# Performance work log

Hardware: AMD Instinct MI355X
Metric: run time of the kernel (lower is better)

## Reference

```python
import jax, jax.numpy as jnp
import numpy as np

H = 2048       # hidden_size
F = 1024       # moe_intermediate_size
E = 32         # n_routed_experts
G = 8          # n_group
TOPK_GROUP = 3
TOP_K = 6      # num_experts_per_tok
N_SHARED = 2
SCALE = 1.0    # routed_scaling_factor
B, S = 1, 2048


def setup_inputs() -> dict:
    key = jax.random.key(0)
    ks = jax.random.split(key, 8)
    std = 0.02
    return {
        "hidden_states": jax.random.normal(ks[0], (B, S, H), dtype=jnp.float32),
        "w_gate": jax.random.normal(ks[1], (E, H), dtype=jnp.float32) * std,
        "wg": jax.random.normal(ks[2], (E, H, F), dtype=jnp.float32) * std,  # stacked gate_proj
        "wu": jax.random.normal(ks[3], (E, H, F), dtype=jnp.float32) * std,  # stacked up_proj
        "wd": jax.random.normal(ks[4], (E, F, H), dtype=jnp.float32) * std,  # stacked down_proj
        "sg": jax.random.normal(ks[5], (N_SHARED * F, H), dtype=jnp.float32) * std,  # shared gate_proj
        "su": jax.random.normal(ks[6], (N_SHARED * F, H), dtype=jnp.float32) * std,  # shared up_proj
        "sd": jax.random.normal(ks[7], (H, N_SHARED * F), dtype=jnp.float32) * std,  # shared down_proj
    }


def reference(hidden_states, w_gate, wg, wu, wd, sg, su, sd):
    b, s, h = hidden_states.shape
    x = hidden_states.reshape(-1, h)                    # [T, H]
    T = x.shape[0]

    # ---- MoEGate (softmax scoring, group_limited_greedy top-k) ----
    logits = x.astype(jnp.float32) @ w_gate.T           # [T, E]
    scores = jax.nn.softmax(logits, axis=-1)
    group_scores = scores.reshape(T, G, E // G).max(axis=-1)          # [T, G]
    _, group_idx = jax.lax.top_k(group_scores, TOPK_GROUP)            # [T, topk_group]
    group_mask = jax.nn.one_hot(group_idx, G, dtype=scores.dtype).sum(axis=1)  # [T, G]
    score_mask = jnp.repeat(group_mask, E // G, axis=-1)              # [T, E]
    tmp_scores = jnp.where(score_mask > 0.5, scores, 0.0)
    topk_weight, topk_idx = jax.lax.top_k(tmp_scores, TOP_K)          # [T, K]
    # norm_topk_prob=True, top_k>1
    topk_weight = topk_weight / (topk_weight.sum(axis=-1, keepdims=True) + 1e-20) * SCALE

    # combine weights per (token, expert): scatter topk weights (indices distinct)
    combine_w = jnp.zeros((T, E), dtype=jnp.float32)
    combine_w = combine_w.at[jnp.arange(T)[:, None], topk_idx].add(topk_weight)

    # ---- routed experts: dense grouped GEMMs, weighted combine ----
    g = jnp.einsum('th,ehf->etf', x, wg)                # [E, T, F]
    u = jnp.einsum('th,ehf->etf', x, wu)                # [E, T, F]
    act = jax.nn.silu(g) * u                            # SiLU gated
    act = act * combine_w.T[:, :, None]                 # fold combine weights before down-proj
    y = jnp.einsum('etf,efh->th', act, wd)              # [T, H]

    # ---- shared experts ----
    shared = (jax.nn.silu(x @ sg.T) * (x @ su.T)) @ sd.T

    return (y + shared).reshape(b, s, h)
```

## Files before the change

### kernel.cpp

```cpp
#include <hip/hip_runtime.h>

#define HD   2048
#define FD   1024
#define NEXP 32
#define TOPK 6
#define TT   2048
#define SDIM 2048
#define NPAIR (TT*TOPK)

typedef __bf16 bf16x8 __attribute__((ext_vector_type(8)));
typedef float  f32x4  __attribute__((ext_vector_type(4)));

#define GLOAD_LDS16(g, l) __builtin_amdgcn_global_load_lds( \
    (const __attribute__((address_space(1))) void*)(g),     \
    (__attribute__((address_space(3))) void*)(l), 16, 0, 0)

#define WAIT_VM3  asm volatile("s_waitcnt vmcnt(3)" ::: "memory")
#define WAIT_VM0  asm volatile("s_waitcnt vmcnt(0)" ::: "memory")
#define BAR() do { __builtin_amdgcn_s_barrier(); } while (0)

__device__ __forceinline__ ushort f2b(float f) {
  __bf16 h = (__bf16)f;
  union { __bf16 h; ushort u; } v; v.h = h;
  return v.u;
// ... 102 lines not shown

__global__ __launch_bounds__(256) void fconv4(
    const float* __restrict__ s0, const float* __restrict__ s1,
    const float* __restrict__ s2, const float* __restrict__ s3,
    ushort* __restrict__ d0, ushort* __restrict__ d1,
    ushort* __restrict__ d2, ushort* __restrict__ d3)
{
  int sel = blockIdx.y;
  const float* in = (sel == 0) ? s0 : (sel == 1) ? s1 : (sel == 2) ? s2 : s3;
  ushort* out = (sel == 0) ? d0 : (sel == 1) ? d1 : (sel == 2) ? d2 : d3;
  int i = blockIdx.x * blockDim.x + threadIdx.x;
  float4 v = ((const float4*)in)[i];
  ((ushort4*)out)[i] = make_ushort4(f2b(v.x), f2b(v.y), f2b(v.z), f2b(v.w));
}

#define TSTR 76
__global__ __launch_bounds__(256) void tconv2(
    const float* __restrict__ in0, const float* __restrict__ in1,
    ushort* __restrict__ out0, ushort* __restrict__ out1, int R, int C)
{
  __shared__ ushort T[64*TSTR];
  const float* inz = blockIdx.z ? in1 : in0;
  ushort* outz = blockIdx.z ? out1 : out0;
  int tiles_c = C >> 6;
  int bt = blockIdx.x;
  int r0 = (bt / tiles_c) << 6;
  int c0 = (bt % tiles_c) << 6;
  const float* src = inz + (size_t)blockIdx.y * R * C;
  ushort* dst = outz + (size_t)blockIdx.y * R * C;
  int t = threadIdx.x;
  int row = (t >> 4) << 2;
  int col4 = (t & 15) << 2;
  float vv[4][4];
  #pragma unroll
  for (int i = 0; i < 4; ++i) {
    float4 v = *(const float4*)(src + (size_t)(r0 + row + i) * C + c0 + col4);
    vv[i][0] = v.x; vv[i][1] = v.y; vv[i][2] = v.z; vv[i][3] = v.w;
  }
  #pragma unroll
  for (int cc = 0; cc < 4; ++cc)
    *(ushort4*)&T[(col4 + cc)*TSTR + row] =
      make_ushort4(f2b(vv[0][cc]), f2b(vv[1][cc]), f2b(vv[2][cc]), f2b(vv[3][cc]));
  __syncthreads();
  #pragma unroll
  for (int p = 0; p < 2; ++p) {
    int item = t + p*256;
    int oc = item >> 3, seg = item & 7;
    ushort4 a = *(const ushort4*)&T[oc*TSTR + seg*8];
    ushort4 b = *(const ushort4*)&T[oc*TSTR + seg*8 + 4];
    ushort* d = dst + (size_t)(c0 + oc) * R + r0 + seg*8;
    *(ushort4*)(d)     = a;
    *(ushort4*)(d + 4) = b;
  }
}

__global__ __launch_bounds__(256) void combine_kernel(
    const ushort* __restrict__ pairout, const int* __restrict__ inv, float* __restrict__ y)
{
  int t = blockIdx.x;
  int h0 = threadIdx.x * 8;
  const int* iv = inv + t*TOPK;
  float* yr = y + (size_t)t * HD + h0;
  float4 y0 = *(const float4*)(yr);
  float4 y1 = *(const float4*)(yr + 4);
  float acc[8] = {y0.x, y0.y, y0.z, y0.w, y1.x, y1.y, y1.z, y1.w};
  #pragma unroll
  for (int r = 0; r < TOPK; ++r) {
    int p = iv[r];
    const ushort* pr = pairout + (size_t)p * HD + h0;
    ushort4 a = *(const ushort4*)(pr);
    ushort4 b = *(const ushort4*)(pr + 4);
    acc[0] += b2f(a.x); acc[1] += b2f(a.y); acc[2] += b2f(a.z); acc[3] += b2f(a.w);
    acc[4] += b2f(b.x); acc[5] += b2f(b.y); acc[6] += b2f(b.z); acc[7] += b2f(b.w);
  }
  *(float4*)(yr)     = make_float4(acc[0], acc[1], acc[2], acc[3]);
  *(float4*)(yr + 4) = make_float4(acc[4], acc[5], acc[6], acc[7]);
}


__global__ __launch_bounds__(512, 4) void gu_routed_b(
    const ushort* __restrict__ xb, const ushort* __restrict__ wgt, const ushort* __restrict__ wut,
    const int* __restrict__ pair_tok, const float* __restrict__ pair_w,
    const int* __restrict__ cnt, const int* __restrict__ offs,
    const int* __restrict__ tl_e, const int* __restrict__ tl_m, const int* __restrict__ ntl,
    ushort* __restrict__ act)
{
  __shared__ ushort A[3][256*32];
  __shared__ ushort Bg[3][64*32];
  __shared__ ushort Bu[3][64*32];

  int nact = ntl[0] * 16;
  int bid = blockIdx.x;
  if (bid >= nact) return;
  int wid = xcd_swz(bid, nact);
  int tile = wid >> 4;
  int nt = wid & 15;
  int e  = tl_e[tile];
  int m0 = tl_m[tile];
  int ce = cnt[e];
  int oe = offs[e];
  int n0 = nt * 64;
  int tid = threadIdx.x, lane = tid & 63, w = tid >> 6;

  int csrc = (lane & 3) ^ ((lane >> 3) & 3);
  const ushort* asrc[2];
  #pragma unroll
  for (int j = 0; j < 2; ++j) {
    int r = (2*w + j)*16 + (lane >> 2);
    int pi = min(m0 + r, ce - 1);
    asrc[j] = xb + (size_t)pair_tok[oe + pi] * HD + csrc * 8;
  }
  int tsel = w >> 2;
  int bw = w & 3;
  const ushort* bsrc = (tsel ? wut : wgt) +
      ((size_t)e * FD + n0 + bw*16 + (lane >> 2)) * HD + csrc * 8;
  ushort* bdst0 = tsel ? &Bu[0][bw*512] : &Bg[0][bw*512];
  ushort* bdst1 = tsel ? &Bu[1][bw*512] : &Bg[1][bw*512];
  ushort* bdst2 = tsel ? &Bu[2][bw*512] : &Bg[2][bw*512];

  int lm = lane & 15, lg = lane >> 4;
  int wr = w >> 1, wc = w & 1;
  int asw = (lm >> 1) & 3;

  f32x4 accg[4][2], accu[4][2];
  #pragma unroll
  for (int m = 0; m < 4; ++m)
    #pragma unroll
    for (int n = 0; n < 2; ++n) { accg[m][n] = f32x4{0,0,0,0}; accu[m][n] = f32x4{0,0,0,0}; }

  #define GUB_ISSUE(T, BUF, BD) do { \
    GLOAD_LDS16(asrc[0] + (T)*32, &A[BUF][(2*w)*512]); \
    GLOAD_LDS16(asrc[1] + (T)*32, &A[BUF][(2*w+1)*512]); \
    GLOAD_LDS16(bsrc + (T)*32, BD); \
  } while (0)
  #define GUB_COMPUTE(BUF) do { \
    bf16x8 a[4], bg[2], bu[2]; \
    _Pragma("unroll") \
    for (int m = 0; m < 4; ++m) \
      a[m] = *(const bf16x8*)&A[BUF][(wr*64 + m*16 + lm)*32 + (lg ^ asw)*8]; \
    _Pragma("unroll") \
    for (int n = 0; n < 2; ++n) { \
      int row = wc*32 + n*16 + lm; \
      bg[n] = *(const bf16x8*)&Bg[BUF][row*32 + (lg ^ asw)*8]; \
      bu[n] = *(const bf16x8*)&Bu[BUF][row*32 + (lg ^ asw)*8]; \
    } \
    __builtin_amdgcn_s_setprio(1); \
    _Pragma("unroll") \
    for (int m = 0; m < 4; ++m) \
      _Pragma("unroll") \
      for (int n = 0; n < 2; ++n) { \
        accg[m][n] = __builtin_amdgcn_mfma_f32_16x16x32_bf16(a[m], bg[n], accg[m][n], 0, 0, 0); \
        accu[m][n] = __builtin_amdgcn_mfma_f32_16x16x32_bf16(a[m], bu[n], accu[m][n], 0, 0, 0); \
      } \
    __builtin_amdgcn_s_setprio(0); \
  } while (0)

  GUB_ISSUE(0, 0, bdst0);
  GUB_ISSUE(1, 1, bdst1);
  WAIT_VM3;
  BAR();

  for (int tt = 0; tt < 20; ++tt) {
    int t = tt * 3;
    GUB_ISSUE(t+2, 2, bdst2); GUB_COMPUTE(0); WAIT_VM3; BAR();
    GUB_ISSUE(t+3, 0, bdst0); GUB_COMPUTE(1); WAIT_VM3; BAR();
    GUB_ISSUE(t+4, 1, bdst1); GUB_COMPUTE(2); WAIT_VM3; BAR();
  }
  GUB_ISSUE(62, 2, bdst2); GUB_COMPUTE(0); WAIT_VM3; BAR();
  GUB_ISSUE(63, 0, bdst0); GUB_COMPUTE(1); WAIT_VM3; BAR();
  GUB_COMPUTE(2); WAIT_VM0; BAR();
  GUB_COMPUTE(0);
  #undef GUB_ISSUE
  #undef GUB_COMPUTE

  #pragma unroll
  for (int m = 0; m < 4; ++m) {
    #pragma unroll
    for (int j = 0; j < 4; ++j) {
      int rl = wr*64 + m*16 + lg*4 + j;
      int pi = m0 + rl;
      if (pi >= ce) continue;
      float pwv = pair_w[oe + pi];
      size_t base = (size_t)(oe + pi) * FD + n0 + wc*32;
      #pragma unroll
      for (int n = 0; n < 2; ++n) {
        float gv = accg[m][n][j];
        float uv = accu[m][n][j];
        float sv = gv / (1.f + __expf(-gv));
        act[base + n*16 + lm] = f2b(sv * uv * pwv);
      }
    }
  }
}

__global__ __launch_bounds__(512, 4) void down_routed_b(
    const ushort* __restrict__ act, const ushort* __restrict__ wdt,
    const int* __restrict__ cnt, const int* __restrict__ offs,
    const int* __restrict__ tl_e, const int* __restrict__ tl_m, const int* __restrict__ ntl,
    ushort* __restrict__ pairout)
{
  __shared__ ushort A[3][256*32];
  __shared__ ushort Bd[3][128*32];

  int nact = ntl[0] * 16;
  int bid = blockIdx.x;
  if (bid >= nact) return;
  int wid = xcd_swz(bid, nact);
  int tile = wid >> 4;
  int nt = wid & 15;
  int e  = tl_e[tile];
  int m0 = tl_m[tile];
  int ce = cnt[e];
  int oe = offs[e];
  int n0 = nt * 128;
  int tid = threadIdx.x, lane = tid & 63, w = tid >> 6;

  int csrc = (lane & 3) ^ ((lane >> 3) & 3);
  const ushort* asrc[2];
  #pragma unroll
  for (int j = 0; j < 2; ++j) {
    int r = (2*w + j)*16 + (lane >> 2);
    int pi = min(m0 + r, ce - 1);
    asrc[j] = act + (size_t)(oe + pi) * FD + csrc * 8;
  }
  const ushort* bsrc = wdt + ((size_t)e * HD + n0 + w*16 + (lane >> 2)) * FD + csrc * 8;

  int lm = lane & 15, lg = lane >> 4;
  int wr = w >> 1, wc = w & 1;
  int asw = (lm >> 1) & 3;

  f32x4 acc[4][4];
  #pragma unroll
  for (int m = 0; m < 4; ++m)
    #pragma unroll
    for (int n = 0; n < 4; ++n) acc[m][n] = f32x4{0,0,0,0};

  #define DNB_ISSUE(T, BUF) do { \
    GLOAD_LDS16(asrc[0] + (T)*32, &A[BUF][(2*w)*512]); \
    GLOAD_LDS16(asrc[1] + (T)*32, &A[BUF][(2*w+1)*512]); \
    GLOAD_LDS16(bsrc + (T)*32, &Bd[BUF][w*512]); \
  } while (0)
  #define DNB_COMPUTE(BUF) do { \
    bf16x8 a[4], b[4]; \
    _Pragma("unroll") \
    for (int m = 0; m < 4; ++m) \
      a[m] = *(const bf16x8*)&A[BUF][(wr*64 + m*16 + lm)*32 + (lg ^ asw)*8]; \
    _Pragma("unroll") \
    for (int n = 0; n < 4; ++n) { \
      int row = wc*64 + n*16 + lm; \
      b[n] = *(const bf16x8*)&Bd[BUF][row*32 + (lg ^ asw)*8]; \
    } \
    __builtin_amdgcn_s_setprio(1); \
    _Pragma("unroll") \
    for (int m = 0; m < 4; ++m) \
      _Pragma("unroll") \
      for (int n = 0; n < 4; ++n) \
        acc[m][n] = __builtin_amdgcn_mfma_f32_16x16x32_bf16(a[m], b[n], acc[m][n], 0, 0, 0); \
    __builtin_amdgcn_s_setprio(0); \
  } while (0)

  DNB_ISSUE(0, 0);
  DNB_ISSUE(1, 1);
  WAIT_VM3;
  BAR();

  for (int tt = 0; tt < 10; ++tt) {
    int t = tt * 3;
    DNB_ISSUE(t+2, 2); DNB_COMPUTE(0); WAIT_VM3; BAR();
    DNB_ISSUE(t+3, 0); DNB_COMPUTE(1); WAIT_VM3; BAR();
    DNB_ISSUE(t+4, 1); DNB_COMPUTE(2); WAIT_VM3; BAR();
  }
  DNB_COMPUTE(0); WAIT_VM0; BAR();
  DNB_COMPUTE(1);
  #undef DNB_ISSUE
  #undef DNB_COMPUTE

  #pragma unroll
  for (int m = 0; m < 4; ++m) {
    #pragma unroll
    for (int j = 0; j < 4; ++j) {
      int rl = wr*64 + m*16 + lg*4 + j;
      int pi = m0 + rl;
      if (pi >= ce) continue;
      size_t base = (size_t)(oe + pi) * HD + n0 + wc*64;
      #pragma unroll
      for (int n = 0; n < 4; ++n)
        pairout[base + n*16 + lm] = f2b(acc[m][n][j]);
    }
  }
}

__global__ __launch_bounds__(512, 4) void shared_gu_b(
    const ushort* __restrict__ xb, const ushort* __restrict__ sgb, const ushort* __restrict__ sub,
    ushort* __restrict__ sact)
{
  __shared__ ushort A[3][256*32];
  __shared__ ushort Bg[3][64*32];
  __shared__ ushort Bu[3][64*32];

  int bid = blockIdx.x;
  int wid = (bid & 7) * 32 + (bid >> 3);
  int mt = wid & 7;
  int nt = wid >> 3;
  int m0 = mt * 256;
  int n0 = nt * 64;
  int tid = threadIdx.x, lane = tid & 63, w = tid >> 6;

  int csrc = (lane & 3) ^ ((lane >> 3) & 3);
  const ushort* asrc[2];
  #pragma unroll
  for (int j = 0; j < 2; ++j) {
    int r = (2*w + j)*16 + (lane >> 2);
    asrc[j] = xb + (size_t)(m0 + r) * HD + csrc * 8;
  }
  int tsel = w >> 2;
  int bw = w & 3;
  const ushort* bsrc = (tsel ? sub : sgb) + (size_t)(n0 + bw*16 + (lane >> 2)) * HD + csrc * 8;
  ushort* bdst0 = tsel ? &Bu[0][bw*512] : &Bg[0][bw*512];
  ushort* bdst1 = tsel ? &Bu[1][bw*512] : &Bg[1][bw*512];
  ushort* bdst2 = tsel ? &Bu[2][bw*512] : &Bg[2][bw*512];

  int lm = lane & 15, lg = lane >> 4;
  int wr = w >> 1, wc = w & 1;
  int asw = (lm >> 1) & 3;

  f32x4 accg[4][2], accu[4][2];
  #pragma unroll
  for (int m = 0; m < 4; ++m)
    #pragma unroll
    for (int n = 0; n < 2; ++n) { accg[m][n] = f32x4{0,0,0,0}; accu[m][n] = f32x4{0,0,0,0}; }

  #define SGB_ISSUE(T, BUF, BD) do { \
    GLOAD_LDS16(asrc[0] + (T)*32, &A[BUF][(2*w)*512]); \
    GLOAD_LDS16(asrc[1] + (T)*32, &A[BUF][(2*w+1)*512]); \
    GLOAD_LDS16(bsrc + (T)*32, BD); \
  } while (0)
  #define SGB_COMPUTE(BUF) do { \
    bf16x8 a[4], bg[2], bu[2]; \
    _Pragma("unroll") \
    for (int m = 0; m < 4; ++m) \
      a[m] = *(const bf16x8*)&A[BUF][(wr*64 + m*16 + lm)*32 + (lg ^ asw)*8]; \
    _Pragma("unroll") \
    for (int n = 0; n < 2; ++n) { \
      int row = wc*32 + n*16 + lm; \
      bg[n] = *(const bf16x8*)&Bg[BUF][row*32 + (lg ^ asw)*8]; \
      bu[n] = *(const bf16x8*)&Bu[BUF][row*32 + (lg ^ asw)*8]; \
    } \
    __builtin_amdgcn_s_setprio(1); \
    _Pragma("unroll") \
    for (int m = 0; m < 4; ++m) \
      _Pragma("unroll") \
      for (int n = 0; n < 2; ++n) { \
        accg[m][n] = __builtin_amdgcn_mfma_f32_16x16x32_bf16(a[m], bg[n], accg[m][n], 0, 0, 0); \
        accu[m][n] = __builtin_amdgcn_mfma_f32_16x16x32_bf16(a[m], bu[n], accu[m][n], 0, 0, 0); \
      } \
    __builtin_amdgcn_s_setprio(0); \
  } while (0)

  SGB_ISSUE(0, 0, bdst0);
  SGB_ISSUE(1, 1, bdst1);
  WAIT_VM3;
  BAR();

  for (int tt = 0; tt < 20; ++tt) {
    int t = tt * 3;
    SGB_ISSUE(t+2, 2, bdst2); SGB_COMPUTE(0); WAIT_VM3; BAR();
    SGB_ISSUE(t+3, 0, bdst0); SGB_COMPUTE(1); WAIT_VM3; BAR();
    SGB_ISSUE(t+4, 1, bdst1); SGB_COMPUTE(2); WAIT_VM3; BAR();
  }
  SGB_ISSUE(62, 2, bdst2); SGB_COMPUTE(0); WAIT_VM3; BAR();
  SGB_ISSUE(63, 0, bdst0); SGB_COMPUTE(1); WAIT_VM3; BAR();
  SGB_COMPUTE(2); WAIT_VM0; BAR();
  SGB_COMPUTE(0);
  #undef SGB_ISSUE
  #undef SGB_COMPUTE

  #pragma unroll
  for (int m = 0; m < 4; ++m) {
    #pragma unroll
    for (int j = 0; j < 4; ++j) {
      int rl = wr*64 + m*16 + lg*4 + j;
      size_t base = (size_t)(m0 + rl) * SDIM + n0 + wc*32;
      #pragma unroll
      for (int n = 0; n < 2; ++n) {
        float gv = accg[m][n][j];
        float uv = accu[m][n][j];
        float sv = gv / (1.f + __expf(-gv));
        sact[base + n*16 + lm] = f2b(sv * uv);
      }
    }
  }
}

__global__ __launch_bounds__(512, 4) void shared_down_b(
    const ushort* __restrict__ sact, const ushort* __restrict__ sdb, float* __restrict__ y)
{
  __shared__ ushort A[3][256*32];
  __shared__ ushort Bd[3][128*32];

  int bid = blockIdx.x;
  int wid = (bid & 7) * 16 + (bid >> 3);
  int mt = wid & 7;
  int nt = wid >> 3;
  int m0 = mt * 256;
  int n0 = nt * 128;
  int tid = threadIdx.x, lane = tid & 63, w = tid >> 6;

  int csrc = (lane & 3) ^ ((lane >> 3) & 3);
  const ushort* asrc[2];
  #pragma unroll
  for (int j = 0; j < 2; ++j) {
    int r = (2*w + j)*16 + (lane >> 2);
    asrc[j] = sact + (size_t)(m0 + r) * SDIM + csrc * 8;
  }
  const ushort* bsrc = sdb + (size_t)(n0 + w*16 + (lane >> 2)) * SDIM + csrc * 8;

  int lm = lane & 15, lg = lane >> 4;
  int wr = w >> 1, wc = w & 1;
  int asw = (lm >> 1) & 3;

  f32x4 acc[4][4];
  #pragma unroll
  for (int m = 0; m < 4; ++m)
    #pragma unroll
    for (int n = 0; n < 4; ++n) acc[m][n] = f32x4{0,0,0,0};

  #define SDB_ISSUE(T, BUF) do { \
    GLOAD_LDS16(asrc[0] + (T)*32, &A[BUF][(2*w)*512]); \
    GLOAD_LDS16(asrc[1] + (T)*32, &A[BUF][(2*w+1)*512]); \
    GLOAD_LDS16(bsrc + (T)*32, &Bd[BUF][w*512]); \
  } while (0)
  #define SDB_COMPUTE(BUF) do { \
    bf16x8 a[4], b[4]; \
    _Pragma("unroll") \
    for (int m = 0; m < 4; ++m) \
      a[m] = *(const bf16x8*)&A[BUF][(wr*64 + m*16 + lm)*32 + (lg ^ asw)*8]; \
    _Pragma("unroll") \
    for (int n = 0; n < 4; ++n) { \
      int row = wc*64 + n*16 + lm; \
      b[n] = *(const bf16x8*)&Bd[BUF][row*32 + (lg ^ asw)*8]; \
    } \
    __builtin_amdgcn_s_setprio(1); \
    _Pragma("unroll") \
    for (int m = 0; m < 4; ++m) \
      _Pragma("unroll") \
      for (int n = 0; n < 4; ++n) \
        acc[m][n] = __builtin_amdgcn_mfma_f32_16x16x32_bf16(a[m], b[n], acc[m][n], 0, 0, 0); \
    __builtin_amdgcn_s_setprio(0); \
  } while (0)

  SDB_ISSUE(0, 0);
  SDB_ISSUE(1, 1);
  WAIT_VM3;
  BAR();

  for (int tt = 0; tt < 20; ++tt) {
    int t = tt * 3;
    SDB_ISSUE(t+2, 2); SDB_COMPUTE(0); WAIT_VM3; BAR();
    SDB_ISSUE(t+3, 0); SDB_COMPUTE(1); WAIT_VM3; BAR();
    SDB_ISSUE(t+4, 1); SDB_COMPUTE(2); WAIT_VM3; BAR();
  }
  SDB_ISSUE(62, 2); SDB_COMPUTE(0); WAIT_VM3; BAR();
  SDB_ISSUE(63, 0); SDB_COMPUTE(1); WAIT_VM3; BAR();
  SDB_COMPUTE(2); WAIT_VM0; BAR();
  SDB_COMPUTE(0);
  #undef SDB_ISSUE
  #undef SDB_COMPUTE

  #pragma unroll
  for (int m = 0; m < 4; ++m) {
    #pragma unroll
    for (int j = 0; j < 4; ++j) {
      int rl = wr*64 + m*16 + lg*4 + j;
      size_t base = (size_t)(m0 + rl) * HD + n0 + wc*64;
      #pragma unroll
      for (int n = 0; n < 4; ++n)
        y[base + n*16 + lm] = acc[m][n][j];
    }
  }
}

extern "C" void kernel_launch(void* const* d_in, const int* in_sizes, int n_in,
                              void* d_out, int out_size, void* d_ws, size_t ws_size,
                              hipStream_t stream) {
  const float* x     = (const float*)d_in[0];
  const float* wgate = (const float*)d_in[1];
  const float* wg    = (const float*)d_in[2];
  const float* wu    = (const float*)d_in[3];
  const float* wd    = (const float*)d_in[4];
  const float* sg    = (const float*)d_in[5];
  const float* su    = (const float*)d_in[6];
  const float* sd    = (const float*)d_in[7];
// ... 17 lines not shown
  ushort* wgt  = (ushort*)(ws + 50331648);
  ushort* wut  = (ushort*)(ws + 184549376);
  ushort* wdt  = (ushort*)(ws + 318767104);
  ushort* sgb  = (ushort*)(ws + 452984832);
  ushort* sub  = (ushort*)(ws + 461373440);
  ushort* sdb  = (ushort*)(ws + 469762048);
  ushort* pairout = wgt;

  hipMemsetAsync(cnt, 0, 512, stream);

  gating_kernel<<<dim3(TT), dim3(64), 0, stream>>>(x, wgate, tidx, tw, cnt);
  scan_kernel<<<dim3(1), dim3(64), 0, stream>>>(cnt, offs, tl_e, tl_m, ntl);
  fill_kernel<<<dim3(48), dim3(256), 0, stream>>>(tidx, tw, offs, curc, ptok, pw, inv);

  fconv4<<<dim3(4096, 4), dim3(256), 0, stream>>>(x, sg, su, sd, xb, sgb, sub, sdb);
  tconv2<<<dim3(512, NEXP, 2), dim3(256), 0, stream>>>(wg, wu, wgt, wut, HD, FD);
  tconv2<<<dim3(512, NEXP, 1), dim3(256), 0, stream>>>(wd, wd, wdt, wdt, FD, HD);

  shared_gu_b<<<dim3(256), dim3(512), 0, stream>>>(xb, sgb, sub, sact);
  shared_down_b<<<dim3(128), dim3(512), 0, stream>>>(sact, sdb, y);
  gu_routed_b<<<dim3(1280), dim3(512), 0, stream>>>(xb, wgt, wut, ptok, pw, cnt, offs,
                                                    tl_e, tl_m, ntl, act);
  down_routed_b<<<dim3(1280), dim3(512), 0, stream>>>(act, wdt, cnt, offs,
                                                      tl_e, tl_m, ntl, pairout);
  combine_kernel<<<dim3(TT), dim3(256), 0, stream>>>(pairout, inv, y);
}
```

Measured before the change: 733.4 us.

## Merge routed/shared GEMMs and wd transpose into heterogeneous mega kernels

Fuses the routed gate/up GEMM, the wd transpose-convert and the shared gate/up GEMM into one launch that dispatches on block index. The routed and shared down GEMMs are likewise merged into a second launch, and the wg/wu transposes now run two jobs per 512-thread block. The aim is to overlap independent memory-bound conversion with compute-bound GEMMs, cut launch gaps, and fill the tail of the routed grid. In exchange, each block holds a union-sized shared pool and register use is set by the heaviest branch, which can lower occupancy for the light transpose blocks.

```diff
diff --git a/kernel.cpp b/kernel.cpp
--- a/kernel.cpp
+++ b/kernel.cpp
@@ -7,6 +7,7 @@
 #define TT   2048
 #define SDIM 2048
 #define NPAIR (TT*TOPK)
+#define TSTR 76
 
 typedef __bf16 bf16x8 __attribute__((ext_vector_type(8)));
 typedef float  f32x4  __attribute__((ext_vector_type(4)));
@@ -140,21 +141,15 @@
   ((ushort4*)out)[i] = make_ushort4(f2b(v.x), f2b(v.y), f2b(v.z), f2b(v.w));
 }
 
-#define TSTR 76
-__global__ __launch_bounds__(256) void tconv2(
-    const float* __restrict__ in0, const float* __restrict__ in1,
-    ushort* __restrict__ out0, ushort* __restrict__ out1, int R, int C)
-{
-  __shared__ ushort T[64*TSTR];
-  const float* inz = blockIdx.z ? in1 : in0;
-  ushort* outz = blockIdx.z ? out1 : out0;
+__device__ __forceinline__ void tconv_job(
+    const float* __restrict__ in, ushort* __restrict__ out,
+    int R, int C, int ey, int bt, int t, ushort* T)
+{
   int tiles_c = C >> 6;
-  int bt = blockIdx.x;
   int r0 = (bt / tiles_c) << 6;
   int c0 = (bt % tiles_c) << 6;
-  const float* src = inz + (size_t)blockIdx.y * R * C;
-  ushort* dst = outz + (size_t)blockIdx.y * R * C;
-  int t = threadIdx.x;
+  const float* src = in + (size_t)ey * R * C;
+  ushort* dst = out + (size_t)ey * R * C;
   int row = (t >> 4) << 2;
   int col4 = (t & 15) << 2;
   float vv[4][4];
@@ -178,6 +173,19 @@
     *(ushort4*)(d)     = a;
     *(ushort4*)(d + 4) = b;
   }
+}
+
+__global__ __launch_bounds__(512) void tconvA(
+    const float* __restrict__ wg, const float* __restrict__ wu,
+    ushort* __restrict__ wgt, ushort* __restrict__ wut)
+{
+  __shared__ ushort T2[2][64*TSTR];
+  int half = threadIdx.x >> 8, t = threadIdx.x & 255;
+  int job = blockIdx.x * 2 + half;
+  const float* in = (job < 16384) ? wg : wu;
+  ushort* out = (job < 16384) ? wgt : wut;
+  int j = job & 16383;
+  tconv_job(in, out, HD, FD, j >> 9, j & 511, t, T2[half]);
 }
 
 __global__ __launch_bounds__(256) void combine_kernel(
@@ -203,405 +211,391 @@
   *(float4*)(yr + 4) = make_float4(acc[4], acc[5], acc[6], acc[7]);
 }
 
-
-__global__ __launch_bounds__(512, 4) void gu_routed_b(
+__global__ __launch_bounds__(512, 4) void mega_gu(
     const ushort* __restrict__ xb, const ushort* __restrict__ wgt, const ushort* __restrict__ wut,
     const int* __restrict__ pair_tok, const float* __restrict__ pair_w,
     const int* __restrict__ cnt, const int* __restrict__ offs,
     const int* __restrict__ tl_e, const int* __restrict__ tl_m, const int* __restrict__ ntl,
-    ushort* __restrict__ act)
-{
-  __shared__ ushort A[3][256*32];
-  __shared__ ushort Bg[3][64*32];
-  __shared__ ushort Bu[3][64*32];
-
-  int nact = ntl[0] * 16;
-  int bid = blockIdx.x;
-  if (bid >= nact) return;
-  int wid = xcd_swz(bid, nact);
-  int tile = wid >> 4;
-  int nt = wid & 15;
-  int e  = tl_e[tile];
-  int m0 = tl_m[tile];
-  int ce = cnt[e];
-  int oe = offs[e];
-  int n0 = nt * 64;
-  int tid = threadIdx.x, lane = tid & 63, w = tid >> 6;
-
-  int csrc = (lane & 3) ^ ((lane >> 3) & 3);
-  const ushort* asrc[2];
-  #pragma unroll
-  for (int j = 0; j < 2; ++j) {
-    int r = (2*w + j)*16 + (lane >> 2);
-    int pi = min(m0 + r, ce - 1);
-    asrc[j] = xb + (size_t)pair_tok[oe + pi] * HD + csrc * 8;
-  }
-  int tsel = w >> 2;
-  int bw = w & 3;
-  const ushort* bsrc = (tsel ? wut : wgt) +
-      ((size_t)e * FD + n0 + bw*16 + (lane >> 2)) * HD + csrc * 8;
-  ushort* bdst0 = tsel ? &Bu[0][bw*512] : &Bg[0][bw*512];
-  ushort* bdst1 = tsel ? &Bu[1][bw*512] : &Bg[1][bw*512];
-  ushort* bdst2 = tsel ? &Bu[2][bw*512] : &Bg[2][bw*512];
-
-  int lm = lane & 15, lg = lane >> 4;
-  int wr = w >> 1, wc = w & 1;
-  int asw = (lm >> 1) & 3;
-
-  f32x4 accg[4][2], accu[4][2];
-  #pragma unroll
-  for (int m = 0; m < 4; ++m)
-    #pragma unroll
-    for (int n = 0; n < 2; ++n) { accg[m][n] = f32x4{0,0,0,0}; accu[m][n] = f32x4{0,0,0,0}; }
-
-  #define GUB_ISSUE(T, BUF, BD) do { \
-    GLOAD_LDS16(asrc[0] + (T)*32, &A[BUF][(2*w)*512]); \
-    GLOAD_LDS16(asrc[1] + (T)*32, &A[BUF][(2*w+1)*512]); \
-    GLOAD_LDS16(bsrc + (T)*32, BD); \
-  } while (0)
-  #define GUB_COMPUTE(BUF) do { \
-    bf16x8 a[4], bg[2], bu[2]; \
-    _Pragma("unroll") \
-    for (int m = 0; m < 4; ++m) \
-      a[m] = *(const bf16x8*)&A[BUF][(wr*64 + m*16 + lm)*32 + (lg ^ asw)*8]; \
-    _Pragma("unroll") \
-    for (int n = 0; n < 2; ++n) { \
-      int row = wc*32 + n*16 + lm; \
-      bg[n] = *(const bf16x8*)&Bg[BUF][row*32 + (lg ^ asw)*8]; \
-      bu[n] = *(const bf16x8*)&Bu[BUF][row*32 + (lg ^ asw)*8]; \
-    } \
-    __builtin_amdgcn_s_setprio(1); \
-    _Pragma("unroll") \
-    for (int m = 0; m < 4; ++m) \
+    ushort* __restrict__ act,
+    const float* __restrict__ wd, ushort* __restrict__ wdt,
+    const ushort* __restrict__ sgb, const ushort* __restrict__ sub, ushort* __restrict__ sact)
+{
+  __shared__ ushort pool[36864];
+  int b = blockIdx.x;
+  int tid = threadIdx.x;
+
+  if (b < 1280) {
+    ushort* Ap  = pool;
+    ushort* Bgp = pool + 24576;
+    ushort* Bup = pool + 30720;
+    int nact = ntl[0] * 16;
+    if (b >= nact) return;
+    int wid = xcd_swz(b, nact);
+    int tile = wid >> 4;
+    int nt = wid & 15;
+    int e  = tl_e[tile];
+    int m0 = tl_m[tile];
+    int ce = cnt[e];
+    int oe = offs[e];
+    int n0 = nt * 64;
+    int lane = tid & 63, w = tid >> 6;
+    int csrc = (lane & 3) ^ ((lane >> 3) & 3);
+    const ushort* asrc0; const ushort* asrc1;
+    {
+      int r = (2*w)*16 + (lane >> 2);
+      asrc0 = xb + (size_t)pair_tok[oe + min(m0 + r,      ce - 1)] * HD + csrc * 8;
+      asrc1 = xb + (size_t)pair_tok[oe + min(m0 + r + 16, ce - 1)] * HD + csrc * 8;
+    }
+    int tsel = w >> 2;
+    int bw = w & 3;
+    const ushort* bsrc = (tsel ? wut : wgt) +
+        ((size_t)e * FD + n0 + bw*16 + (lane >> 2)) * HD + csrc * 8;
+    ushort* bbase = (tsel ? Bup : Bgp) + bw*512;
+    int lm = lane & 15, lg = lane >> 4;
+    int wr = w >> 1, wc = w & 1;
+    int asw = (lm >> 1) & 3;
+
+    f32x4 accg[4][2], accu[4][2];
+    #pragma unroll
+    for (int m = 0; m < 4; ++m)
+      #pragma unroll
+      for (int n = 0; n < 2; ++n) { accg[m][n] = f32x4{0,0,0,0}; accu[m][n] = f32x4{0,0,0,0}; }
+
+    #define GUB_ISSUE(T, BUF) do { \
+      GLOAD_LDS16(asrc0 + (T)*32, Ap + (BUF)*8192 + (2*w)*512); \
+      GLOAD_LDS16(asrc1 + (T)*32, Ap + (BUF)*8192 + (2*w+1)*512); \
+      GLOAD_LDS16(bsrc + (T)*32, bbase + (BUF)*2048); \
+    } while (0)
+    #define GUB_COMPUTE(BUF) do { \
+      bf16x8 a[4], bg[2], bu[2]; \
+      _Pragma("unroll") \
+      for (int m = 0; m < 4; ++m) \
+        a[m] = *(const bf16x8*)(Ap + (BUF)*8192 + (wr*64 + m*16 + lm)*32 + (lg ^ asw)*8); \
       _Pragma("unroll") \
       for (int n = 0; n < 2; ++n) { \
-        accg[m][n] = __builtin_amdgcn_mfma_f32_16x16x32_bf16(a[m], bg[n], accg[m][n], 0, 0, 0); \
-        accu[m][n] = __builtin_amdgcn_mfma_f32_16x16x32_bf16(a[m], bu[n], accu[m][n], 0, 0, 0); \
+        int row = wc*32 + n*16 + lm; \
+        bg[n] = *(const bf16x8*)(Bgp + (BUF)*2048 + row*32 + (lg ^ asw)*8); \
+        bu[n] = *(const bf16x8*)(Bup + (BUF)*2048 + row*32 + (lg ^ asw)*8); \
       } \
-    __builtin_amdgcn_s_setprio(0); \
-  } while (0)
-
-  GUB_ISSUE(0, 0, bdst0);
-  GUB_ISSUE(1, 1, bdst1);
-  WAIT_VM3;
-  BAR();
-
-  for (int tt = 0; tt < 20; ++tt) {
-    int t = tt * 3;
-    GUB_ISSUE(t+2, 2, bdst2); GUB_COMPUTE(0); WAIT_VM3; BAR();
-    GUB_ISSUE(t+3, 0, bdst0); GUB_COMPUTE(1); WAIT_VM3; BAR();
-    GUB_ISSUE(t+4, 1, bdst1); GUB_COMPUTE(2); WAIT_VM3; BAR();
-  }
-  GUB_ISSUE(62, 2, bdst2); GUB_COMPUTE(0); WAIT_VM3; BAR();
-  GUB_ISSUE(63, 0, bdst0); GUB_COMPUTE(1); WAIT_VM3; BAR();
-  GUB_COMPUTE(2); WAIT_VM0; BAR();
-  GUB_COMPUTE(0);
-  #undef GUB_ISSUE
-  #undef GUB_COMPUTE
-
-  #pragma unroll
-  for (int m = 0; m < 4; ++m) {
-    #pragma unroll
-    for (int j = 0; j < 4; ++j) {
-      int rl = wr*64 + m*16 + lg*4 + j;
-      int pi = m0 + rl;
-      if (pi >= ce) continue;
-      float pwv = pair_w[oe + pi];
-      size_t base = (size_t)(oe + pi) * FD + n0 + wc*32;
-      #pragma unroll
-      for (int n = 0; n < 2; ++n) {
-        float gv = accg[m][n][j];
-        float uv = accu[m][n][j];
-        float sv = gv / (1.f + __expf(-gv));
-        act[base + n*16 + lm] = f2b(sv * uv * pwv);
+      __builtin_amdgcn_s_setprio(1); \
+      _Pragma("unroll") \
+      for (int m = 0; m < 4; ++m) \
+        _Pragma("unroll") \
+        for (int n = 0; n < 2; ++n) { \
+          accg[m][n] = __builtin_amdgcn_mfma_f32_16x16x32_bf16(a[m], bg[n], accg[m][n], 0, 0, 0); \
+          accu[m][n] = __builtin_amdgcn_mfma_f32_16x16x32_bf16(a[m], bu[n], accu[m][n], 0, 0, 0); \
+        } \
+      __builtin_amdgcn_s_setprio(0); \
+    } while (0)
+
+    GUB_ISSUE(0, 0);
+    GUB_ISSUE(1, 1);
+    WAIT_VM3;
+    BAR();
+    for (int tt = 0; tt < 20; ++tt) {
+      int t = tt * 3;
+      GUB_ISSUE(t+2, 2); GUB_COMPUTE(0); WAIT_VM3; BAR();
+      GUB_ISSUE(t+3, 0); GUB_COMPUTE(1); WAIT_VM3; BAR();
+      GUB_ISSUE(t+4, 1); GUB_COMPUTE(2); WAIT_VM3; BAR();
+    }
+    GUB_ISSUE(62, 2); GUB_COMPUTE(0); WAIT_VM3; BAR();
+    GUB_ISSUE(63, 0); GUB_COMPUTE(1); WAIT_VM3; BAR();
+    GUB_COMPUTE(2); WAIT_VM0; BAR();
+    GUB_COMPUTE(0);
+    #undef GUB_ISSUE
+    #undef GUB_COMPUTE
+
+    #pragma unroll
+    for (int m = 0; m < 4; ++m) {
+      #pragma unroll
+      for (int j = 0; j < 4; ++j) {
+        int rl = wr*64 + m*16 + lg*4 + j;
+        int pi = m0 + rl;
+        if (pi >= ce) continue;
+        float pwv = pair_w[oe + pi];
+        size_t base = (size_t)(oe + pi) * FD + n0 + wc*32;
+        #pragma unroll
+        for (int n = 0; n < 2; ++n) {
+          float gv = accg[m][n][j];
+          float uv = accu[m][n][j];
+          float sv = gv / (1.f + __expf(-gv));
+          act[base + n*16 + lm] = f2b(sv * uv * pwv);
+        }
       }
     }
-  }
-}
-
-__global__ __launch_bounds__(512, 4) void down_routed_b(
+  } else if (b < 1280 + 8192) {
+    ushort* T = pool + (tid >> 8) * (64*TSTR);
+    int t = tid & 255;
+    int job = (b - 1280) * 2 + (tid >> 8);
+    tconv_job(wd, wdt, FD, HD, job >> 9, job & 511, t, T);
+  } else {
+    ushort* Ap  = pool;
+    ushort* Bgp = pool + 24576;
+    ushort* Bup = pool + 30720;
+    int sbid = b - (1280 + 8192);
+    int wid = (sbid & 7) * 32 + (sbid >> 3);
+    int mt = wid & 7;
+    int nt = wid >> 3;
+    int m0 = mt * 256;
+    int n0 = nt * 64;
+    int lane = tid & 63, w = tid >> 6;
+    int csrc = (lane & 3) ^ ((lane >> 3) & 3);
+    const ushort* asrc0; const ushort* asrc1;
+    {
+      int r = (2*w)*16 + (lane >> 2);
+      asrc0 = xb + (size_t)(m0 + r)      * HD + csrc * 8;
+      asrc1 = xb + (size_t)(m0 + r + 16) * HD + csrc * 8;
+    }
+    int tsel = w >> 2;
+    int bw = w & 3;
+    const ushort* bsrc = (tsel ? sub : sgb) + (size_t)(n0 + bw*16 + (lane >> 2)) * HD + csrc * 8;
+    ushort* bbase = (tsel ? Bup : Bgp) + bw*512;
+    int lm = lane & 15, lg = lane >> 4;
+    int wr = w >> 1, wc = w & 1;
+    int asw = (lm >> 1) & 3;
+
+    f32x4 accg[4][2], accu[4][2];
+    #pragma unroll
+    for (int m = 0; m < 4; ++m)
+      #pragma unroll
+      for (int n = 0; n < 2; ++n) { accg[m][n] = f32x4{0,0,0,0}; accu[m][n] = f32x4{0,0,0,0}; }
+
+    #define SGB_ISSUE(T, BUF) do { \
+      GLOAD_LDS16(asrc0 + (T)*32, Ap + (BUF)*8192 + (2*w)*512); \
+      GLOAD_LDS16(asrc1 + (T)*32, Ap + (BUF)*8192 + (2*w+1)*512); \
+      GLOAD_LDS16(bsrc + (T)*32, bbase + (BUF)*2048); \
+    } while (0)
+    #define SGB_COMPUTE(BUF) do { \
+      bf16x8 a[4], bg[2], bu[2]; \
+      _Pragma("unroll") \
+      for (int m = 0; m < 4; ++m) \
+        a[m] = *(const bf16x8*)(Ap + (BUF)*8192 + (wr*64 + m*16 + lm)*32 + (lg ^ asw)*8); \
+      _Pragma("unroll") \
+      for (int n = 0; n < 2; ++n) { \
+        int row = wc*32 + n*16 + lm; \
+        bg[n] = *(const bf16x8*)(Bgp + (BUF)*2048 + row*32 + (lg ^ asw)*8); \
+        bu[n] = *(const bf16x8*)(Bup + (BUF)*2048 + row*32 + (lg ^ asw)*8); \
+      } \
+      __builtin_amdgcn_s_setprio(1); \
+      _Pragma("unroll") \
+      for (int m = 0; m < 4; ++m) \
+        _Pragma("unroll") \
+        for (int n = 0; n < 2; ++n) { \
+          accg[m][n] = __builtin_amdgcn_mfma_f32_16x16x32_bf16(a[m], bg[n], accg[m][n], 0, 0, 0); \
+          accu[m][n] = __builtin_amdgcn_mfma_f32_16x16x32_bf16(a[m], bu[n], accu[m][n], 0, 0, 0); \
+        } \
+      __builtin_amdgcn_s_setprio(0); \
+    } while (0)
+
+    SGB_ISSUE(0, 0);
+    SGB_ISSUE(1, 1);
+    WAIT_VM3;
+    BAR();
+    for (int tt = 0; tt < 20; ++tt) {
+      int t = tt * 3;
+      SGB_ISSUE(t+2, 2); SGB_COMPUTE(0); WAIT_VM3; BAR();
+      SGB_ISSUE(t+3, 0); SGB_COMPUTE(1); WAIT_VM3; BAR();
+      SGB_ISSUE(t+4, 1); SGB_COMPUTE(2); WAIT_VM3; BAR();
+    }
+    SGB_ISSUE(62, 2); SGB_COMPUTE(0); WAIT_VM3; BAR();
+    SGB_ISSUE(63, 0); SGB_COMPUTE(1); WAIT_VM3; BAR();
+    SGB_COMPUTE(2); WAIT_VM0; BAR();
+    SGB_COMPUTE(0);
+    #undef SGB_ISSUE
+    #undef SGB_COMPUTE
+
+    #pragma unroll
+    for (int m = 0; m < 4; ++m) {
+      #pragma unroll
+      for (int j = 0; j < 4; ++j) {
+        int rl = wr*64 + m*16 + lg*4 + j;
+        size_t base = (size_t)(m0 + rl) * SDIM + n0 + wc*32;
+        #pragma unroll
+        for (int n = 0; n < 2; ++n) {
+          float gv = accg[m][n][j];
+          float uv = accu[m][n][j];
+          float sv = gv / (1.f + __expf(-gv));
+          sact[base + n*16 + lm] = f2b(sv * uv);
+        }
+      }
+    }
+  }
+}
+
+__global__ __launch_bounds__(512, 4) void mega_dn(
     const ushort* __restrict__ act, const ushort* __restrict__ wdt,
     const int* __restrict__ cnt, const int* __restrict__ offs,
     const int* __restrict__ tl_e, const int* __restrict__ tl_m, const int* __restrict__ ntl,
-    ushort* __restrict__ pairout)
-{
-  __shared__ ushort A[3][256*32];
-  __shared__ ushort Bd[3][128*32];
-
-  int nact = ntl[0] * 16;
-  int bid = blockIdx.x;
-  if (bid >= nact) return;
-  int wid = xcd_swz(bid, nact);
-  int tile = wid >> 4;
-  int nt = wid & 15;
-  int e  = tl_e[tile];
-  int m0 = tl_m[tile];
-  int ce = cnt[e];
-  int oe = offs[e];
-  int n0 = nt * 128;
-  int tid = threadIdx.x, lane = tid & 63, w = tid >> 6;
-
-  int csrc = (lane & 3) ^ ((lane >> 3) & 3);
-  const ushort* asrc[2];
-  #pragma unroll
-  for (int j = 0; j < 2; ++j) {
-    int r = (2*w + j)*16 + (lane >> 2);
-    int pi = min(m0 + r, ce - 1);
-    asrc[j] = act + (size_t)(oe + pi) * FD + csrc * 8;
-  }
-  const ushort* bsrc = wdt + ((size_t)e * HD + n0 + w*16 + (lane >> 2)) * FD + csrc * 8;
-
-  int lm = lane & 15, lg = lane >> 4;
-  int wr = w >> 1, wc = w & 1;
-  int asw = (lm >> 1) & 3;
-
-  f32x4 acc[4][4];
-  #pragma unroll
-  for (int m = 0; m < 4; ++m)
-    #pragma unroll
-    for (int n = 0; n < 4; ++n) acc[m][n] = f32x4{0,0,0,0};
-
-  #define DNB_ISSUE(T, BUF) do { \
-    GLOAD_LDS16(asrc[0] + (T)*32, &A[BUF][(2*w)*512]); \
-    GLOAD_LDS16(asrc[1] + (T)*32, &A[BUF][(2*w+1)*512]); \
-    GLOAD_LDS16(bsrc + (T)*32, &Bd[BUF][w*512]); \
-  } while (0)
-  #define DNB_COMPUTE(BUF) do { \
-    bf16x8 a[4], b[4]; \
-    _Pragma("unroll") \
-    for (int m = 0; m < 4; ++m) \
-      a[m] = *(const bf16x8*)&A[BUF][(wr*64 + m*16 + lm)*32 + (lg ^ asw)*8]; \
-    _Pragma("unroll") \
-    for (int n = 0; n < 4; ++n) { \
-      int row = wc*64 + n*16 + lm; \
-      b[n] = *(const bf16x8*)&Bd[BUF][row*32 + (lg ^ asw)*8]; \
-    } \
-    __builtin_amdgcn_s_setprio(1); \
-    _Pragma("unroll") \
-    for (int m = 0; m < 4; ++m) \
-      _Pragma("unroll") \
-      for (int n = 0; n < 4; ++n) \
-        acc[m][n] = __builtin_amdgcn_mfma_f32_16x16x32_bf16(a[m], b[n], acc[m][n], 0, 0, 0); \
-    __builtin_amdgcn_s_setprio(0); \
-  } while (0)
-
-  DNB_ISSUE(0, 0);
-  DNB_ISSUE(1, 1);
-  WAIT_VM3;
-  BAR();
-
-  for (int tt = 0; tt < 10; ++tt) {
-    int t = tt * 3;
-    DNB_ISSUE(t+2, 2); DNB_COMPUTE(0); WAIT_VM3; BAR();
-    DNB_ISSUE(t+3, 0); DNB_COMPUTE(1); WAIT_VM3; BAR();
-    DNB_ISSUE(t+4, 1); DNB_COMPUTE(2); WAIT_VM3; BAR();
-  }
-  DNB_COMPUTE(0); WAIT_VM0; BAR();
-  DNB_COMPUTE(1);
-  #undef DNB_ISSUE
-  #undef DNB_COMPUTE
-
-  #pragma unroll
-  for (int m = 0; m < 4; ++m) {
-    #pragma unroll
-    for (int j = 0; j < 4; ++j) {
-      int rl = wr*64 + m*16 + lg*4 + j;
-      int pi = m0 + rl;
-      if (pi >= ce) continue;
-      size_t base = (size_t)(oe + pi) * HD + n0 + wc*64;
-      #pragma unroll
-      for (int n = 0; n < 4; ++n)
-        pairout[base + n*16 + lm] = f2b(acc[m][n][j]);
-    }
-  }
-}
-
-__global__ __launch_bounds__(512, 4) void shared_gu_b(
-    const ushort* __restrict__ xb, const ushort* __restrict__ sgb, const ushort* __restrict__ sub,
-    ushort* __restrict__ sact)
-{
-  __shared__ ushort A[3][256*32];
-  __shared__ ushort Bg[3][64*32];
-  __shared__ ushort Bu[3][64*32];
-
-  int bid = blockIdx.x;
-  int wid = (bid & 7) * 32 + (bid >> 3);
-  int mt = wid & 7;
-  int nt = wid >> 3;
-  int m0 = mt * 256;
-  int n0 = nt * 64;
-  int tid = threadIdx.x, lane = tid & 63, w = tid >> 6;
-
-  int csrc = (lane & 3) ^ ((lane >> 3) & 3);
-  const ushort* asrc[2];
-  #pragma unroll
-  for (int j = 0; j < 2; ++j) {
-    int r = (2*w + j)*16 + (lane >> 2);
-    asrc[j] = xb + (size_t)(m0 + r) * HD + csrc * 8;
-  }
-  int tsel = w >> 2;
-  int bw = w & 3;
-  const ushort* bsrc = (tsel ? sub : sgb) + (size_t)(n0 + bw*16 + (lane >> 2)) * HD + csrc * 8;
-  ushort* bdst0 = tsel ? &Bu[0][bw*512] : &Bg[0][bw*512];
-  ushort* bdst1 = tsel ? &Bu[1][bw*512] : &Bg[1][bw*512];
-  ushort* bdst2 = tsel ? &Bu[2][bw*512] : &Bg[2][bw*512];
-
-  int lm = lane & 15, lg = lane >> 4;
-  int wr = w >> 1, wc = w & 1;
-  int asw = (lm >> 1) & 3;
-
-  f32x4 accg[4][2], accu[4][2];
-  #pragma unroll
-  for (int m = 0; m < 4; ++m)
-    #pragma unroll
-    for (int n = 0; n < 2; ++n) { accg[m][n] = f32x4{0,0,0,0}; accu[m][n] = f32x4{0,0,0,0}; }
-
-  #define SGB_ISSUE(T, BUF, BD) do { \
-    GLOAD_LDS16(asrc[0] + (T)*32, &A[BUF][(2*w)*512]); \
-    GLOAD_LDS16(asrc[1] + (T)*32, &A[BUF][(2*w+1)*512]); \
-    GLOAD_LDS16(bsrc + (T)*32, BD); \
-  } while (0)
-  #define SGB_COMPUTE(BUF) do { \
-    bf16x8 a[4], bg[2], bu[2]; \
-    _Pragma("unroll") \
-    for (int m = 0; m < 4; ++m) \
-      a[m] = *(const bf16x8*)&A[BUF][(wr*64 + m*16 + lm)*32 + (lg ^ asw)*8]; \
-    _Pragma("unroll") \
-    for (int n = 0; n < 2; ++n) { \
-      int row = wc*32 + n*16 + lm; \
-      bg[n] = *(const bf16x8*)&Bg[BUF][row*32 + (lg ^ asw)*8]; \
-      bu[n] = *(const bf16x8*)&Bu[BUF][row*32 + (lg ^ asw)*8]; \
-    } \
-    __builtin_amdgcn_s_setprio(1); \
-    _Pragma("unroll") \
-    for (int m = 0; m < 4; ++m) \
-      _Pragma("unroll") \
-      for (int n = 0; n < 2; ++n) { \
-        accg[m][n] = __builtin_amdgcn_mfma_f32_16x16x32_bf16(a[m], bg[n], accg[m][n], 0, 0, 0); \
-        accu[m][n] = __builtin_amdgcn_mfma_f32_16x16x32_bf16(a[m], bu[n], accu[m][n], 0, 0, 0); \
+    ushort* __restrict__ pairout,
+    const ushort* __restrict__ sact, const ushort* __restrict__ sdb, float* __restrict__ y)
+{
+  __shared__ ushort pool[36864];
+  int b = blockIdx.x;
+  int tid = threadIdx.x;
+
+  if (b < 1280) {
+    ushort* Ap  = pool;
+    ushort* Bdp = pool + 24576;
+    int nact = ntl[0] * 16;
+    if (b >= nact) return;
+    int wid = xcd_swz(b, nact);
+    int tile = wid >> 4;
+    int nt = wid & 15;
+    int e  = tl_e[tile];
+    int m0 = tl_m[tile];
+    int ce = cnt[e];
+    int oe = offs[e];
+    int n0 = nt * 128;
+    int lane = tid & 63, w = tid >> 6;
+    int csrc = (lane & 3) ^ ((lane >> 3) & 3);
+    const ushort* asrc0; const ushort* asrc1;
+    {
+      int r = (2*w)*16 + (lane >> 2);
+      asrc0 = act + (size_t)(oe + min(m0 + r,      ce - 1)) * FD + csrc * 8;
+      asrc1 = act + (size_t)(oe + min(m0 + r + 16, ce - 1)) * FD + csrc * 8;
+    }
+    const ushort* bsrc = wdt + ((size_t)e * HD + n0 + w*16 + (lane >> 2)) * FD + csrc * 8;
+    int lm = lane & 15, lg = lane >> 4;
+    int wr = w >> 1, wc = w & 1;
+    int asw = (lm >> 1) & 3;
+
+    f32x4 acc[4][4];
+    #pragma unroll
+    for (int m = 0; m < 4; ++m)
+      #pragma unroll
+      for (int n = 0; n < 4; ++n) acc[m][n] = f32x4{0,0,0,0};
+
+    #define DNB_ISSUE(T, BUF) do { \
+      GLOAD_LDS16(asrc0 + (T)*32, Ap + (BUF)*8192 + (2*w)*512); \
+      GLOAD_LDS16(asrc1 + (T)*32, Ap + (BUF)*8192 + (2*w+1)*512); \
+      GLOAD_LDS16(bsrc + (T)*32, Bdp + (BUF)*4096 + w*512); \
+    } while (0)
+    #define DNB_COMPUTE(BUF) do { \
+      bf16x8 a[4], bvv[4]; \
+      _Pragma("unroll") \
+      for (int m = 0; m < 4; ++m) \
+        a[m] = *(const bf16x8*)(Ap + (BUF)*8192 + (wr*64 + m*16 + lm)*32 + (lg ^ asw)*8); \
+      _Pragma("unroll") \
+      for (int n = 0; n < 4; ++n) { \
+        int row = wc*64 + n*16 + lm; \
+        bvv[n] = *(const bf16x8*)(Bdp + (BUF)*4096 + row*32 + (lg ^ asw)*8); \
       } \
-    __builtin_amdgcn_s_setprio(0); \
-  } while (0)
-
-  SGB_ISSUE(0, 0, bdst0);
-  SGB_ISSUE(1, 1, bdst1);
-  WAIT_VM3;
-  BAR();
-
-  for (int tt = 0; tt < 20; ++tt) {
-    int t = tt * 3;
-    SGB_ISSUE(t+2, 2, bdst2); SGB_COMPUTE(0); WAIT_VM3; BAR();
-    SGB_ISSUE(t+3, 0, bdst0); SGB_COMPUTE(1); WAIT_VM3; BAR();
-    SGB_ISSUE(t+4, 1, bdst1); SGB_COMPUTE(2); WAIT_VM3; BAR();
-  }
-  SGB_ISSUE(62, 2, bdst2); SGB_COMPUTE(0); WAIT_VM3; BAR();
-  SGB_ISSUE(63, 0, bdst0); SGB_COMPUTE(1); WAIT_VM3; BAR();
-  SGB_COMPUTE(2); WAIT_VM0; BAR();
-  SGB_COMPUTE(0);
-  #undef SGB_ISSUE
-  #undef SGB_COMPUTE
-
-  #pragma unroll
-  for (int m = 0; m < 4; ++m) {
-    #pragma unroll
-    for (int j = 0; j < 4; ++j) {
-      int rl = wr*64 + m*16 + lg*4 + j;
-      size_t base = (size_t)(m0 + rl) * SDIM + n0 + wc*32;
-      #pragma unroll
-      for (int n = 0; n < 2; ++n) {
-        float gv = accg[m][n][j];
-        float uv = accu[m][n][j];
-        float sv = gv / (1.f + __expf(-gv));
-        sact[base + n*16 + lm] = f2b(sv * uv);
+      __builtin_amdgcn_s_setprio(1); \
+      _Pragma("unroll") \
+      for (int m = 0; m < 4; ++m) \
+        _Pragma("unroll") \
+        for (int n = 0; n < 4; ++n) \
+          acc[m][n] = __builtin_amdgcn_mfma_f32_16x16x32_bf16(a[m], bvv[n], acc[m][n], 0, 0, 0); \
+      __builtin_amdgcn_s_setprio(0); \
+    } while (0)
+
+    DNB_ISSUE(0, 0);
+    DNB_ISSUE(1, 1);
+    WAIT_VM3;
+    BAR();
+    for (int tt = 0; tt < 10; ++tt) {
+      int t = tt * 3;
+      DNB_ISSUE(t+2, 2); DNB_COMPUTE(0); WAIT_VM3; BAR();
+      DNB_ISSUE(t+3, 0); DNB_COMPUTE(1); WAIT_VM3; BAR();
+      DNB_ISSUE(t+4, 1); DNB_COMPUTE(2); WAIT_VM3; BAR();
+    }
+    DNB_COMPUTE(0); WAIT_VM0; BAR();
+    DNB_COMPUTE(1);
+    #undef DNB_ISSUE
+    #undef DNB_COMPUTE
+
+    #pragma unroll
+    for (int m = 0; m < 4; ++m) {
+      #pragma unroll
+      for (int j = 0; j < 4; ++j) {
+        int rl = wr*64 + m*16 + lg*4 + j;
+        int pi = m0 + rl;
+        if (pi >= ce) continue;
+        size_t base = (size_t)(oe + pi) * HD + n0 + wc*64;
+        #pragma unroll
+        for (int n = 0; n < 4; ++n)
+          pairout[base + n*16 + lm] = f2b(acc[m][n][j]);
       }
     }
-  }
-}
-
-__global__ __launch_bounds__(512, 4) void shared_down_b(
-    const ushort* __restrict__ sact, const ushort* __restrict__ sdb, float* __restrict__ y)
-{
-  __shared__ ushort A[3][256*32];
-  __shared__ ushort Bd[3][128*32];
-
-  int bid = blockIdx.x;
-  int wid = (bid & 7) * 16 + (bid >> 3);
-  int mt = wid & 7;
-  int nt = wid >> 3;
-  int m0 = mt * 256;
-  int n0 = nt * 128;
-  int tid = threadIdx.x, lane = tid & 63, w = tid >> 6;
-
-  int csrc = (lane & 3) ^ ((lane >> 3) & 3);
-  const ushort* asrc[2];
-  #pragma unroll
-  for (int j = 0; j < 2; ++j) {
-    int r = (2*w + j)*16 + (lane >> 2);
-    asrc[j] = sact + (size_t)(m0 + r) * SDIM + csrc * 8;
-  }
-  const ushort* bsrc = sdb + (size_t)(n0 + w*16 + (lane >> 2)) * SDIM + csrc * 8;
-
-  int lm = lane & 15, lg = lane >> 4;
-  int wr = w >> 1, wc = w & 1;
-  int asw = (lm >> 1) & 3;
-
-  f32x4 acc[4][4];
-  #pragma unroll
-  for (int m = 0; m < 4; ++m)
-    #pragma unroll
-    for (int n = 0; n < 4; ++n) acc[m][n] = f32x4{0,0,0,0};
-
-  #define SDB_ISSUE(T, BUF) do { \
-    GLOAD_LDS16(asrc[0] + (T)*32, &A[BUF][(2*w)*512]); \
-    GLOAD_LDS16(asrc[1] + (T)*32, &A[BUF][(2*w+1)*512]); \
-    GLOAD_LDS16(bsrc + (T)*32, &Bd[BUF][w*512]); \
-  } while (0)
-  #define SDB_COMPUTE(BUF) do { \
-    bf16x8 a[4], b[4]; \
-    _Pragma("unroll") \
-    for (int m = 0; m < 4; ++m) \
-      a[m] = *(const bf16x8*)&A[BUF][(wr*64 + m*16 + lm)*32 + (lg ^ asw)*8]; \
-    _Pragma("unroll") \
-    for (int n = 0; n < 4; ++n) { \
-      int row = wc*64 + n*16 + lm; \
-      b[n] = *(const bf16x8*)&Bd[BUF][row*32 + (lg ^ asw)*8]; \
-    } \
-    __builtin_amdgcn_s_setprio(1); \
-    _Pragma("unroll") \
-    for (int m = 0; m < 4; ++m) \
-      _Pragma("unroll") \
-      for (int n = 0; n < 4; ++n) \
-        acc[m][n] = __builtin_amdgcn_mfma_f32_16x16x32_bf16(a[m], b[n], acc[m][n], 0, 0, 0); \
-    __builtin_amdgcn_s_setprio(0); \
-  } while (0)
-
-  SDB_ISSUE(0, 0);
-  SDB_ISSUE(1, 1);
-  WAIT_VM3;
-  BAR();
-
-  for (int tt = 0; tt < 20; ++tt) {
-    int t = tt * 3;
-    SDB_ISSUE(t+2, 2); SDB_COMPUTE(0); WAIT_VM3; BAR();
-    SDB_ISSUE(t+3, 0); SDB_COMPUTE(1); WAIT_VM3; BAR();
-    SDB_ISSUE(t+4, 1); SDB_COMPUTE(2); WAIT_VM3; BAR();
-  }
-  SDB_ISSUE(62, 2); SDB_COMPUTE(0); WAIT_VM3; BAR();
-  SDB_ISSUE(63, 0); SDB_COMPUTE(1); WAIT_VM3; BAR();
-  SDB_COMPUTE(2); WAIT_VM0; BAR();
-  SDB_COMPUTE(0);
-  #undef SDB_ISSUE
-  #undef SDB_COMPUTE
-
-  #pragma unroll
-  for (int m = 0; m < 4; ++m) {
-    #pragma unroll
-    for (int j = 0; j < 4; ++j) {
-      int rl = wr*64 + m*16 + lg*4 + j;
-      size_t base = (size_t)(m0 + rl) * HD + n0 + wc*64;
-      #pragma unroll
-      for (int n = 0; n < 4; ++n)
-        y[base + n*16 + lm] = acc[m][n][j];
+  } else {
+    ushort* Ap  = pool;
+    ushort* Bdp = pool + 24576;
+    int sbid = b - 1280;
+    int wid = (sbid & 7) * 16 + (sbid >> 3);
+    int mt = wid & 7;
+    int nt = wid >> 3;
+    int m0 = mt * 256;
+    int n0 = nt * 128;
+    int lane = tid & 63, w = tid >> 6;
+    int csrc = (lane & 3) ^ ((lane >> 3) & 3);
+    const ushort* asrc0; const ushort* asrc1;
+    {
+      int r = (2*w)*16 + (lane >> 2);
+      asrc0 = sact + (size_t)(m0 + r)      * SDIM + csrc * 8;
+      asrc1 = sact + (size_t)(m0 + r + 16) * SDIM + csrc * 8;
+    }
+    const ushort* bsrc = sdb + (size_t)(n0 + w*16 + (lane >> 2)) * SDIM + csrc * 8;
+    int lm = lane & 15, lg = lane >> 4;
+    int wr = w >> 1, wc = w & 1;
+    int asw = (lm >> 1) & 3;
+
+    f32x4 acc[4][4];
+    #pragma unroll
+    for (int m = 0; m < 4; ++m)
+      #pragma unroll
+      for (int n = 0; n < 4; ++n) acc[m][n] = f32x4{0,0,0,0};
+
+    #define SDB_ISSUE(T, BUF) do { \
+      GLOAD_LDS16(asrc0 + (T)*32, Ap + (BUF)*8192 + (2*w)*512); \
+      GLOAD_LDS16(asrc1 + (T)*32, Ap + (BUF)*8192 + (2*w+1)*512); \
+      GLOAD_LDS16(bsrc + (T)*32, Bdp + (BUF)*4096 + w*512); \
+    } while (0)
+    #define SDB_COMPUTE(BUF) do { \
+      bf16x8 a[4], bvv[4]; \
+      _Pragma("unroll") \
+      for (int m = 0; m < 4; ++m) \
+        a[m] = *(const bf16x8*)(Ap + (BUF)*8192 + (wr*64 + m*16 + lm)*32 + (lg ^ asw)*8); \
+      _Pragma("unroll") \
+      for (int n = 0; n < 4; ++n) { \
+        int row = wc*64 + n*16 + lm; \
+        bvv[n] = *(const bf16x8*)(Bdp + (BUF)*4096 + row*32 + (lg ^ asw)*8); \
+      } \
+      __builtin_amdgcn_s_setprio(1); \
+      _Pragma("unroll") \
+      for (int m = 0; m < 4; ++m) \
+        _Pragma("unroll") \
+        for (int n = 0; n < 4; ++n) \
+          acc[m][n] = __builtin_amdgcn_mfma_f32_16x16x32_bf16(a[m], bvv[n], acc[m][n], 0, 0, 0); \
+      __builtin_amdgcn_s_setprio(0); \
+    } while (0)
+
+    SDB_ISSUE(0, 0);
+    SDB_ISSUE(1, 1);
+    WAIT_VM3;
+    BAR();
+    for (int tt = 0; tt < 20; ++tt) {
+      int t = tt * 3;
+      SDB_ISSUE(t+2, 2); SDB_COMPUTE(0); WAIT_VM3; BAR();
+      SDB_ISSUE(t+3, 0); SDB_COMPUTE(1); WAIT_VM3; BAR();
+      SDB_ISSUE(t+4, 1); SDB_COMPUTE(2); WAIT_VM3; BAR();
+    }
+    SDB_ISSUE(62, 2); SDB_COMPUTE(0); WAIT_VM3; BAR();
+    SDB_ISSUE(63, 0); SDB_COMPUTE(1); WAIT_VM3; BAR();
+    SDB_COMPUTE(2); WAIT_VM0; BAR();
+    SDB_COMPUTE(0);
+    #undef SDB_ISSUE
+    #undef SDB_COMPUTE
+
+    #pragma unroll
+    for (int m = 0; m < 4; ++m) {
+      #pragma unroll
+      for (int j = 0; j < 4; ++j) {
+        int rl = wr*64 + m*16 + lg*4 + j;
+        size_t base = (size_t)(m0 + rl) * HD + n0 + wc*64;
+        #pragma unroll
+        for (int n = 0; n < 4; ++n)
+          y[base + n*16 + lm] = acc[m][n][j];
+      }
     }
   }
 }
@@ -649,14 +643,12 @@
   fill_kernel<<<dim3(48), dim3(256), 0, stream>>>(tidx, tw, offs, curc, ptok, pw, inv);
 
   fconv4<<<dim3(4096, 4), dim3(256), 0, stream>>>(x, sg, su, sd, xb, sgb, sub, sdb);
-  tconv2<<<dim3(512, NEXP, 2), dim3(256), 0, stream>>>(wg, wu, wgt, wut, HD, FD);
-  tconv2<<<dim3(512, NEXP, 1), dim3(256), 0, stream>>>(wd, wd, wdt, wdt, FD, HD);
-
-  shared_gu_b<<<dim3(256), dim3(512), 0, stream>>>(xb, sgb, sub, sact);
-  shared_down_b<<<dim3(128), dim3(512), 0, stream>>>(sact, sdb, y);
-  gu_routed_b<<<dim3(1280), dim3(512), 0, stream>>>(xb, wgt, wut, ptok, pw, cnt, offs,
-                                                    tl_e, tl_m, ntl, act);
-  down_routed_b<<<dim3(1280), dim3(512), 0, stream>>>(act, wdt, cnt, offs,
-                                                      tl_e, tl_m, ntl, pairout);
+  tconvA<<<dim3(16384), dim3(512), 0, stream>>>(wg, wu, wgt, wut);
+
+  mega_gu<<<dim3(1280 + 8192 + 256), dim3(512), 0, stream>>>(
+      xb, wgt, wut, ptok, pw, cnt, offs, tl_e, tl_m, ntl, act,
+      wd, wdt, sgb, sub, sact);
+  mega_dn<<<dim3(1280 + 128), dim3(512), 0, stream>>>(
+      act, wdt, cnt, offs, tl_e, tl_m, ntl, pairout, sact, sdb, y);
   combine_kernel<<<dim3(TT), dim3(256), 0, stream>>>(pairout, inv, y);
 }
```

After: 655.1 us (median of 2 runs). 1.12x faster.
